# Kernel optimization log

Hardware: AMD Instinct MI355X
Metric: run time of the kernel (lower is better)

Reference implementation:

```python
import jax, jax.numpy as jnp
import numpy as np
from functools import partial

IN_DIM = 128
NUM_HEADS = 8
DOWN_DIM = IN_DIM // 2          # 64
HEAD_DIM = DOWN_DIM // NUM_HEADS  # 8
MID = max(1, DOWN_DIM // 16)    # 4 (gate_reduce=16)
DIL = 3
BN_EPS = 1e-5


def conv2d(x, w, padding=0, dilation=1):
    # x: [B,C,H,W], w: [O,I,kh,kw]
    return jax.lax.conv_general_dilated(
        x, w, window_strides=(1, 1),
        padding=[(padding, padding), (padding, padding)],
        rhs_dilation=(dilation, dilation),
        dimension_numbers=("NCHW", "OIHW", "NCHW"))


def batchnorm(x, gamma, beta, mean, var):
    # inference-mode BN over channel dim
    scale = (gamma / jnp.sqrt(var + BN_EPS))[None, :, None, None]
    shift = (beta - mean * gamma / jnp.sqrt(var + BN_EPS))[None, :, None, None]
    return x * scale + shift


def complex_l2_norm(z, eps=1e-6):
    denom = jnp.sqrt(jnp.sum(z.real ** 2 + z.imag ** 2, axis=-1, keepdims=True) + eps)
    return z / denom


def complex_softmax(z):
    return jax.lax.complex(jax.nn.softmax(z.real, axis=-1),
                           jax.nn.softmax(z.imag, axis=-1))


def setup_inputs() -> dict:
    key = jax.random.key(0)
    ks = jax.random.split(key, 6)
    B, H, W = 8, 128, 128
    inp = {}
    inp["x"] = jax.random.normal(ks[0], (B, IN_DIM, H, W), dtype=jnp.float32)
    inp["conv_w"] = jax.random.normal(ks[1], (DOWN_DIM, IN_DIM, 3, 3), dtype=jnp.float32) * 0.02
    inp["bn1_g"] = jnp.ones((DOWN_DIM,), jnp.float32)
    inp["bn1_b"] = jnp.zeros((DOWN_DIM,), jnp.float32)
    inp["bn1_m"] = jnp.zeros((DOWN_DIM,), jnp.float32)
    inp["bn1_v"] = jnp.ones((DOWN_DIM,), jnp.float32)
    inp["cg1_w"] = jax.random.normal(ks[2], (MID, DOWN_DIM, 1, 1), dtype=jnp.float32) * 0.1
    inp["cg1_b"] = jnp.zeros((MID,), jnp.float32)
    inp["cgbn_g"] = jnp.ones((MID,), jnp.float32)
    inp["cgbn_b"] = jnp.zeros((MID,), jnp.float32)
    inp["cgbn_m"] = jnp.zeros((MID,), jnp.float32)
    inp["cgbn_v"] = jnp.ones((MID,), jnp.float32)
    inp["cg2_w"] = jax.random.normal(ks[3], (DOWN_DIM, MID, 1, 1), dtype=jnp.float32) * 0.1
    inp["cg2_b"] = jnp.zeros((DOWN_DIM,), jnp.float32)
    inp["tau"] = jnp.ones((NUM_HEADS, 1, 1), jnp.float32) * (HEAD_DIM ** -0.5)
    return inp


def reference(x, conv_w, bn1_g, bn1_b, bn1_m, bn1_v,
              cg1_w, cg1_b, cgbn_g, cgbn_b, cgbn_m, cgbn_v,
              cg2_w, cg2_b, tau):
    B, C, H, W = x.shape
    # reduce branch: dilated 3x3 conv -> BN -> GELU (exact, matching torch nn.GELU)
    feat = conv2d(x, conv_w, padding=DIL, dilation=DIL)
    feat = batchnorm(feat, bn1_g, bn1_b, bn1_m, bn1_v)
    feat = jax.nn.gelu(feat, approximate=False)

    # q=k=v=g = fft2(feat) (torch computes four identical FFTs; same math)
    F2 = jnp.fft.fft2(feat.astype(jnp.float32), axes=(-2, -1))  # complex64 [B,64,H,W]
    N = H * W
    qkv = F2.reshape(B, NUM_HEADS, HEAD_DIM, N)  # b h d (H W)
    q = complex_l2_norm(qkv)
    k = complex_l2_norm(qkv)
    v = qkv
    # attn: [b,h,d,d] — tiny; contraction over N
    attn = jnp.einsum("bhdn,bhen->bhde", q, jnp.conj(k)) * tau
    attn = complex_softmax(attn)
    out_f = jnp.einsum("bhde,bhen->bhdn", attn, v)
    out_f = out_f.reshape(B, DOWN_DIM, H, W)
    out_f = jnp.abs(jnp.fft.ifft2(out_f, axes=(-2, -1)))

    # gated branch on g = F2
    gr = F2.real
    cg = conv2d(gr, cg1_w) + cg1_b[None, :, None, None]
    cg = batchnorm(cg, cgbn_g, cgbn_b, cgbn_m, cgbn_v)
    cg = jax.nn.gelu(cg, approximate=False)
    cg = conv2d(cg, cg2_w) + cg2_b[None, :, None, None]
    cg = jax.nn.sigmoid(cg)
    gate = cg * F2  # real gate times complex spectrum
    gate = jnp.abs(jnp.fft.ifft2(gate, axes=(-2, -1)))

    y = jnp.concatenate([out_f, gate], axis=1)
    return y + x
```

## Files before the change

### kernel.cpp

```cpp
#include <hip/hip_runtime.h>
#include <hip/hip_bf16.h>
#include <math.h>

#define NB 8
#define CIN 128
#define CDN 64
#define NPIX 16384
#define NHEADS 8
#define HDIM 8

typedef __attribute__((ext_vector_type(8))) short bf16x8;
typedef __attribute__((ext_vector_type(4))) float f32x4;
typedef __attribute__((ext_vector_type(8))) unsigned short u16x8;

struct alignas(8) c2 { float x, y; };

__device__ inline c2 cadd(c2 a, c2 b){ return {a.x+b.x, a.y+b.y}; }
__device__ inline c2 csub(c2 a, c2 b){ return {a.x-b.x, a.y-b.y}; }
__device__ inline c2 cmul(c2 a, c2 b){ return {a.x*b.x - a.y*b.y, a.x*b.y + a.y*b.x}; }
__device__ inline c2 shfl2(c2 v, int m){ return { __shfl_xor(v.x, m, 64), __shfl_xor(v.y, m, 64) }; }
__device__ inline float gelu_exact(float v){ return 0.5f*v*(1.f + erff(v*0.70710678118654752f)); }
__device__ inline unsigned short f2bf(float f){
  __hip_bfloat16 h = __float2bfloat16(f);
  return *reinterpret_cast<unsigned short*>(&h);
}
__device__ inline float bf2f(unsigned short u){ return __uint_as_float((unsigned)u << 16); }

struct Tw { c2 t0; c2 t[6]; };
__device__ inline void tw_init(Tw& w, int t){
  float sn, cs;
  sincosf(-6.283185307179586f * (float)t * (1.f/128.f), &sn, &cs); w.t0 = {cs, sn};
  #pragma unroll
  for (int i = 0; i < 6; ++i) {
    int sp = 32 >> i;
    int j = t & (sp-1);
    sincosf(-3.141592653589793f * (float)j / (float)sp, &sn, &cs);
    w.t[i] = {cs, sn};
  }
}
__device__ inline void fft128_fwd(c2& a, c2& b, int t, const Tw& w){
  c2 s = cadd(a,b), d = csub(a,b);
  a = s; b = cmul(d, w.t0);
  #pragma unroll
  for (int i = 0; i < 6; ++i) {
    int sp = 32 >> i;
    c2 oa = shfl2(a, sp), ob = shfl2(b, sp);
    c2 tw = w.t[i];
    if (t & sp) { a = cmul(csub(oa,a), tw); b = cmul(csub(ob,b), tw); }
    else        { a = cadd(a,oa);           b = cadd(b,ob); }
  }
}
__device__ inline void fft128_inv(c2& a, c2& b, int t, const Tw& w){
  #pragma unroll
  for (int i = 5; i >= 0; --i) {
    int sp = 32 >> i;
    c2 tw = {w.t[i].x, -w.t[i].y};
    c2 oa = shfl2(a, sp), ob = shfl2(b, sp);
    if (t & sp) { a = csub(oa, cmul(a, tw)); b = csub(ob, cmul(b, tw)); }
    else        { a = cadd(a, cmul(oa, tw)); b = cadd(b, cmul(ob, tw)); }
  }
  c2 t0c = {w.t0.x, -w.t0.y};
  c2 wb = cmul(b, t0c);
  b = csub(a, wb);
  a = cadd(a, wb);
}

__device__ inline void gload_lds16(const void* g, void* l){
  __builtin_amdgcn_global_load_lds(
      (const __attribute__((address_space(1))) unsigned int*)g,
      (__attribute__((address_space(3))) unsigned int*)l, 16, 0, 0);
}

__device__ inline int colmap8(int wv, int i){
  if (wv == 0) return i;
  if (wv == 1) return 8 + i;
  if (wv == 2) return i < 4 ? 16 + i : 24 + i;
  if (wv == 3) return 20 + i;
  if (wv < 8) { int a = wv - 4; return i < 4 ? 32 + 4*a + i : 56 - 4*a + i; }
  int a = wv - 8; return i < 4 ? 64 + 4*a + i : 120 - 4*a + i;
}

__global__ __launch_bounds__(256) void k_prep(const float* __restrict__ x, unsigned short* __restrict__ xT,
                                              const float* __restrict__ w, unsigned short* __restrict__ wP){
  if (blockIdx.x < 512) {
    int b = blockIdx.x >> 6;
    int px = (blockIdx.x & 63)*256 + threadIdx.x;
    const float* xb = x + (size_t)b*CIN*NPIX + px;
    #pragma unroll 2
    for (int ci0 = 0; ci0 < 128; ci0 += 8) {
      u16x8 v;
      #pragma unroll
      for (int j = 0; j < 8; ++j) v[j] = f2bf(xb[(size_t)(ci0+j)*NPIX]);
      int cc = ci0 >> 5;
      *(u16x8*)(xT + (((size_t)(b*4+cc)*NPIX + px)*32 + (ci0 & 31))) = v;
    }
  } else {
    int idx = (blockIdx.x - 512)*256 + threadIdx.x;
    if (idx >= 4*9*64*32) return;
    int cc  = idx / 18432;
    int r   = idx - cc*18432;
    int tap = r / 2048;
    int r2  = r - tap*2048;
    int co  = r2 >> 5;
    int cil = r2 & 31;
    int ci  = cc*32 + cil;
    wP[idx] = f2bf(w[(co*CIN + ci)*9 + tap]);
  }
}

__global__ __launch_bounds__(256) void k_conv(const unsigned short* __restrict__ xT,
    const unsigned short* __restrict__ wP,
    const float* __restrict__ bg, const float* __restrict__ bbeta,
    const float* __restrict__ bm, const float* __restrict__ bv,
    const float* __restrict__ w1,
    unsigned short* __restrict__ feat, float* __restrict__ u){
  __shared__ __align__(16) unsigned short sX[512*32];
  __shared__ float w1s[256];
  const int tid = threadIdx.x;
  const int flat = blockIdx.x + (blockIdx.y << 4) + (blockIdx.z << 7);
  const int half = (flat >> 3) & 1;
  const int tf   = (flat & 7) | ((flat >> 4) << 3);
  const int x0 = (tf & 7) * 16;
  const int y0 = ((tf >> 3) & 7) * 16;
  const int bb = tf >> 6;
  const int coBase = half*32;
  const int wv  = tid >> 6;
  const int l   = tid & 63;
  const int l15 = l & 15;
  const int g   = l >> 4;

  w1s[tid] = w1[tid];

  const bool interior = (x0 >= 16) && (x0 <= 96) && (y0 >= 16) && (y0 <= 96);

  f32x4 acc[2][4];
  #pragma unroll
  for (int m=0;m<2;++m)
    #pragma unroll
    for (int n=0;n<4;++n) acc[m][n] = {0.f,0.f,0.f,0.f};

  const int ko = g*8;

  for (int cc = 0; cc < 4; ++cc) {
    __syncthreads();
    const unsigned short* xcc = xT + ((size_t)(bb*4 + cc))*NPIX*32;
    if (interior) {
      #pragma unroll
      for (int k = 0; k < 8; ++k) {
        int blk = k*4 + wv;
        int idx = blk*64 + l;
        int p = idx >> 2, i = idx & 3;
        int pc = p < 484 ? p : 483;
        int py = pc / 22, px = pc - py*22;
        int gpix = (y0-3+py)*128 + (x0-3+px);
        int sg = i ^ ((p >> 1) & 3);
        const unsigned short* srcp = xcc + (size_t)gpix*32 + sg*8;
        gload_lds16(srcp, (char*)sX + blk*1024);
      }
    } else {
      #pragma unroll
      for (int k = 0; k < 8; ++k) {
        int idx = k*256 + tid;
        int p = idx >> 2, i = idx & 3;
        u16x8 v = {0,0,0,0,0,0,0,0};
        if (p < 484) {
          int py = p / 22, px = p - py*22;
          int gy = y0-3+py, gx = x0-3+px;
          if ((unsigned)gy < 128u && (unsigned)gx < 128u) {
            int sg = i ^ ((p >> 1) & 3);
            v = *(const u16x8*)(xcc + (size_t)(gy*128+gx)*32 + sg*8);
          }
        }
        *(u16x8*)((char*)sX + idx*16) = v;
      }
    }
    __syncthreads();

    const unsigned short* wcc = wP + cc*18432;
    for (int tap = 0; tap < 9; ++tap) {
      int dy = (tap/3)*3, dx = (tap - (tap/3)*3)*3;
      const unsigned short* wt = wcc + tap*2048;
      bf16x8 a[2], b[4];
      #pragma unroll
      for (int m = 0; m < 2; ++m)
        a[m] = *reinterpret_cast<const bf16x8*>(wt + (coBase + m*16 + l15)*32 + ko);
      #pragma unroll
      for (int n = 0; n < 4; ++n) {
        int p = (wv*4 + n + dy)*22 + l15 + dx;
        b[n] = *reinterpret_cast<const bf16x8*>(&sX[p*32 + ((g ^ ((p >> 1) & 3)) << 3)]);
      }
      #pragma unroll
      for (int m = 0; m < 2; ++m)
        #pragma unroll
        for (int n = 0; n < 4; ++n)
          acc[m][n] = __builtin_amdgcn_mfma_f32_16x16x32_bf16(a[m], b[n], acc[m][n], 0, 0, 0);
    }
  }

  float up[4][4];
  #pragma unroll
  for (int n=0;n<4;++n)
    #pragma unroll
    for (int m2=0;m2<4;++m2) up[n][m2] = 0.f;

  #pragma unroll
  for (int m = 0; m < 2; ++m) {
    #pragma unroll
    for (int r = 0; r < 4; ++r) {
      int co = coBase + m*16 + g*4 + r;
      float sc = bg[co] * rsqrtf(bv[co] + 1e-5f);
      float sh = bbeta[co] - bm[co]*sc;
      float wv4[4];
      #pragma unroll
      for (int m2 = 0; m2 < 4; ++m2) wv4[m2] = w1s[m2*64 + co];
      #pragma unroll
      for (int n = 0; n < 4; ++n) {
        int py = wv*4 + n;
        float v = gelu_exact(acc[m][n][r]*sc + sh);
        feat[((size_t)(bb*CDN + co)*128 + (y0+py))*128 + x0 + l15] = f2bf(v);
        #pragma unroll
        for (int m2 = 0; m2 < 4; ++m2) up[n][m2] += wv4[m2]*v;
      }
    }
  }
  #pragma unroll
  for (int n=0;n<4;++n)
    #pragma unroll
    for (int m2=0;m2<4;++m2) {
      up[n][m2] += __shfl_xor(up[n][m2], 16, 64);
      up[n][m2] += __shfl_xor(up[n][m2], 32, 64);
    }
  if (g == 0) {
    #pragma unroll
    for (int n = 0; n < 4; ++n) {
      int py = y0 + wv*4 + n;
      #pragma unroll
      for (int m2 = 0; m2 < 4; ++m2)
        u[((size_t)((bb*2 + half)*4 + m2))*NPIX + py*128 + x0 + l15] = up[n][m2];
    }
  }
}

__global__ __launch_bounds__(256) void k_attn1(const unsigned short* __restrict__ feat, float* __restrict__ part){
  int bh = blockIdx.x, ck = blockIdx.y;
  int b = bh >> 3, h = bh & 7;
  const unsigned short* f = feat + (size_t)(b*CDN + h*HDIM)*NPIX;
  float acc[36];
  #pragma unroll
  for (int i=0;i<36;++i) acc[i]=0.f;
  for (int p = ck*2048 + threadIdx.x; p < (ck+1)*2048; p += 256) {
    float v[8];
    #pragma unroll
    for (int d=0; d<8; ++d) v[d] = bf2f(f[d*NPIX + p]);
    int i = 0;
    #pragma unroll
    for (int d=0; d<8; ++d)
      #pragma unroll
      for (int e=0; e<=d; ++e) acc[i++] += v[d]*v[e];
  }
  #pragma unroll
  for (int i=0;i<36;++i)
    #pragma unroll
    for (int off=32; off; off>>=1) acc[i] += __shfl_xor(acc[i], off, 64);
  __shared__ float red[4][36];
  int wave = threadIdx.x >> 6, lane = threadIdx.x & 63;
  if (lane == 0) {
    #pragma unroll
    for (int i=0;i<36;++i) red[wave][i] = acc[i];
  }
  __syncthreads();
  if (threadIdx.x < 36)
    part[(bh*8+ck)*36 + threadIdx.x] =
      red[0][threadIdx.x]+red[1][threadIdx.x]+red[2][threadIdx.x]+red[3][threadIdx.x];
}

__global__ __launch_bounds__(256) void k_outf(const unsigned short* __restrict__ feat, const float* __restrict__ part,
                                              const float* __restrict__ tau,
                                              const float* __restrict__ x, float* __restrict__ out){
  int bh = blockIdx.x; int b = bh >> 3, h = bh & 7;
  int p = blockIdx.y*256 + threadIdx.x;
  __shared__ float A[64];
  __shared__ float Gm[36];
  if (threadIdx.x < 36) {
    float s = 0.f;
    #pragma unroll
    for (int k = 0; k < 8; ++k) s += part[(bh*8+k)*36 + threadIdx.x];
    Gm[threadIdx.x] = s;
  }
  __syncthreads();
  if (threadIdx.x == 0) {
    float G[8][8];
    int c=0;
    for (int d=0;d<8;++d) for(int e=0;e<=d;++e){
      float s = Gm[c]; G[d][e]=s; G[e][d]=s; ++c;
    }
    float nrm[8];
    for (int d=0;d<8;++d) nrm[d] = sqrtf(16384.f*G[d][d] + 1e-6f);
    float tv = tau[h];
    for (int d=0;d<8;++d) {
      float row[8]; float mx = -1e30f;
      for (int e=0;e<8;++e){ row[e] = tv*16384.f*G[d][e]/(nrm[d]*nrm[e]); mx = fmaxf(mx,row[e]); }
      float s=0.f;
      for (int e=0;e<8;++e){ row[e] = expf(row[e]-mx); s += row[e]; }
      for (int e=0;e<8;++e) A[d*8+e] = row[e]/s;
    }
  }
  __syncthreads();
  const unsigned short* f = feat + (size_t)(b*CDN + h*HDIM)*NPIX;
  float v[8];
  #pragma unroll
  for (int e=0;e<8;++e) v[e] = bf2f(f[e*NPIX + p]);
  float im = 0.f;
  #pragma unroll
  for (int e=0;e<8;++e) im += v[e];
  im *= 0.125f;
  #pragma unroll
  for (int d=0;d<8;++d){
    float re = 0.f;
    #pragma unroll
    for (int e=0;e<8;++e) re += A[d*8+e]*v[e];
    size_t o = ((size_t)(b*CIN + h*HDIM + d))*NPIX + p;
    out[o] = sqrtf(re*re + im*im) + x[o];
  }
}

__global__ __launch_bounds__(512) void k_ufft(const float* __restrict__ u,
    const float* __restrict__ b1,
    const float* __restrict__ gg, const float* __restrict__ gbeta,
    const float* __restrict__ gm, const float* __restrict__ gv,
    float* __restrict__ mid){
  __shared__ c2 T[64*129];
  int b = blockIdx.x >> 2, m = blockIdx.x & 3;
  int tid = threadIdx.x, wv = tid >> 6, t = tid & 63;
  Tw w; tw_init(w, t);
  const float* src0 = u + (size_t)((b*2+0)*4+m)*NPIX;
  const float* src1 = u + (size_t)((b*2+1)*4+m)*NPIX;
  c2 ra[16], rb[16];
  #pragma unroll
  for (int i = 0; i < 16; ++i) {
    int y = wv*16 + i;
    ra[i] = {src0[y*128 + t] + src1[y*128 + t], 0.f};
    rb[i] = {src0[y*128 + t + 64] + src1[y*128 + t + 64], 0.f};
  }
  #pragma unroll
  for (int i = 0; i < 16; ++i) fft128_fwd(ra[i], rb[i], t, w);
  c2 ca[16], cb[16];
  if (wv < 4) {
    #pragma unroll
    for (int i = 0; i < 16; ++i) {
      int y = wv*16 + i;
      T[y*129 + t] = ra[i]; T[y*129 + t + 64] = rb[i];
    }
  }
  __syncthreads();
  #pragma unroll
  for (int i = 0; i < 16; ++i) ca[i] = T[t*129 + wv*16 + i];
  __syncthreads();
  if (wv >= 4) {
    #pragma unroll
    for (int i = 0; i < 16; ++i) {
      int y = (wv-4)*16 + i;
      T[y*129 + t] = ra[i]; T[y*129 + t + 64] = rb[i];
    }
  }
  __syncthreads();
  #pragma unroll
  for (int i = 0; i < 16; ++i) cb[i] = T[t*129 + wv*16 + i];
  #pragma unroll
  for (int i = 0; i < 16; ++i) fft128_fwd(ca[i], cb[i], t, w);
  float sc = gg[m]*rsqrtf(gv[m]+1e-5f);
  float sh = gbeta[m] - gm[m]*sc;
  float bb1 = b1[m];
  float* md = mid + (size_t)(b*4+m)*NPIX;
  #pragma unroll
  for (int i = 0; i < 16; ++i) {
    int kx = wv*16 + i;
    md[kx*128 + t]      = gelu_exact((ca[i].x + bb1)*sc + sh);
    md[kx*128 + t + 64] = gelu_exact((cb[i].x + bb1)*sc + sh);
  }
}

__global__ __launch_bounds__(256) void k_gmap(const float* __restrict__ mid, const float* __restrict__ w2,
                                              const float* __restrict__ b2, unsigned* __restrict__ gPack){
  __shared__ float w2s[256], b2s[64];
  w2s[threadIdx.x] = w2[threadIdx.x];
  if (threadIdx.x < 64) b2s[threadIdx.x] = b2[threadIdx.x];
  __syncthreads();
  int b = blockIdx.x >> 6;
  int k = (blockIdx.x & 63)*256 + threadIdx.x;
  const float* md = mid + (size_t)b*4*NPIX + k;
  float m0 = md[0], m1 = md[NPIX], m2 = md[2*NPIX], m3 = md[3*NPIX];
  unsigned* gp = gPack + (size_t)b*32*NPIX + k;
  #pragma unroll 8
  for (int cp = 0; cp < 32; ++cp) {
    float slo = b2s[cp]    + w2s[cp*4]*m0    + w2s[cp*4+1]*m1    + w2s[cp*4+2]*m2    + w2s[cp*4+3]*m3;
    float shi = b2s[cp+32] + w2s[(cp+32)*4]*m0 + w2s[(cp+32)*4+1]*m1 + w2s[(cp+32)*4+2]*m2 + w2s[(cp+32)*4+3]*m3;
    slo = 1.f/(1.f+expf(-slo));
    shi = 1.f/(1.f+expf(-shi));
    gp[(size_t)cp*NPIX] = ((unsigned)f2bf(shi) << 16) | (unsigned)f2bf(slo);
  }
}

__global__ __launch_bounds__(1024)
void k_fused(const unsigned short* __restrict__ feat, const unsigned* __restrict__ gPack,
             const float* __restrict__ x, float* __restrict__ out){
  __shared__ c2 T[128*129];
  int ib = blockIdx.x;
  int b = ib >> 5, c = ib & 31;
  int tid = threadIdx.x, wv = tid >> 6, t = tid & 63;
  Tw w; tw_init(w, t);
  int ta = __brev((64 - (__brev(t) >> 26)) & 63) >> 26;
  const unsigned short* srcA = feat + (size_t)(b*CDN + c)*NPIX;
  const unsigned short* srcB = feat + (size_t)(b*CDN + c + 32)*NPIX;
  const unsigned* gp = gPack + (size_t)(b*32 + c)*NPIX;

  c2 ra[8], rb[8];
  #pragma unroll
  for (int i = 0; i < 8; ++i) {
    int y = wv*8 + i;
    ra[i] = {bf2f(srcA[y*128 + t]),      bf2f(srcB[y*128 + t])};
    rb[i] = {bf2f(srcA[y*128 + t + 64]), bf2f(srcB[y*128 + t + 64])};
  }
  #pragma unroll
  for (int i = 0; i < 8; ++i) fft128_fwd(ra[i], rb[i], t, w);
  #pragma unroll
  for (int i = 0; i < 8; ++i) {
    int y = wv*8 + i;
    T[y*129 + t] = ra[i]; T[y*129 + t + 64] = rb[i];
  }
  __syncthreads();
  c2 ca[8], cb[8];
  #pragma unroll
  for (int i = 0; i < 8; ++i) {
    int s = colmap8(wv, i);
    ca[i] = T[t*129 + s];
    cb[i] = T[(t+64)*129 + s];
  }
  unsigned gwa[8], gwb[8];
  #pragma unroll
  for (int i = 0; i < 8; ++i) {
    int s = colmap8(wv, i);
    gwa[i] = gp[s*128 + t];
    gwb[i] = gp[s*128 + 64 + t];
  }
  #pragma unroll
  for (int i = 0; i < 8; ++i) fft128_fwd(ca[i], cb[i], t, w);

  #define GUN(w_, lo_, hi_) float lo_ = __uint_as_float((w_) << 16); float hi_ = __uint_as_float((w_) & 0xffff0000u);
  #define CPAIR(I, J) { \
    GUN(gwa[I], g1aI, g2aI); GUN(gwb[I], g1bI, g2bI); \
    GUN(gwa[J], g1aJ, g2aJ); GUN(gwb[J], g1bJ, g2bJ); \
    c2 paI = { __shfl(ca[J].x, ta, 64), -__shfl(ca[J].y, ta, 64) }; \
    c2 paJ = { __shfl(ca[I].x, ta, 64), -__shfl(ca[I].y, ta, 64) }; \
    c2 pbI = { __shfl_xor(cb[J].x, 63, 64), -__shfl_xor(cb[J].y, 63, 64) }; \
    c2 pbJ = { __shfl_xor(cb[I].x, 63, 64), -__shfl_xor(cb[I].y, 63, 64) }; \
    float gsaI=0.5f*(g1aI+g2aI), gdaI=0.5f*(g1aI-g2aI); \
    float gsaJ=0.5f*(g1aJ+g2aJ), gdaJ=0.5f*(g1aJ-g2aJ); \
    float gsbI=0.5f*(g1bI+g2bI), gdbI=0.5f*(g1bI-g2bI); \
    float gsbJ=0.5f*(g1bJ+g2bJ), gdbJ=0.5f*(g1bJ-g2bJ); \
    ca[I] = { gsaI*ca[I].x + gdaI*paI.x, gsaI*ca[I].y + gdaI*paI.y }; \
    ca[J] = { gsaJ*ca[J].x + gdaJ*paJ.x, gsaJ*ca[J].y + gdaJ*paJ.y }; \
    cb[I] = { gsbI*cb[I].x + gdbI*pbI.x, gsbI*cb[I].y + gdbI*pbI.y }; \
    cb[J] = { gsbJ*cb[J].x + gdbJ*pbJ.x, gsbJ*cb[J].y + gdbJ*pbJ.y }; \
  }
  #define CSELF(I) { \
    GUN(gwa[I], g1aI, g2aI); GUN(gwb[I], g1bI, g2bI); \
    c2 paI = { __shfl(ca[I].x, ta, 64), -__shfl(ca[I].y, ta, 64) }; \
    c2 pbI = { __shfl_xor(cb[I].x, 63, 64), -__shfl_xor(cb[I].y, 63, 64) }; \
    float gsaI=0.5f*(g1aI+g2aI), gdaI=0.5f*(g1aI-g2aI); \
    float gsbI=0.5f*(g1bI+g2bI), gdbI=0.5f*(g1bI-g2bI); \
    ca[I] = { gsaI*ca[I].x + gdaI*paI.x, gsaI*ca[I].y + gdaI*paI.y }; \
    cb[I] = { gsbI*cb[I].x + gdbI*pbI.x, gsbI*cb[I].y + gdbI*pbI.y }; \
  }
  if (wv == 0) {
    CSELF(0); CSELF(1);
    CPAIR(2,3); CPAIR(4,7); CPAIR(5,6);
  } else {
    CPAIR(0,7); CPAIR(1,6); CPAIR(2,5); CPAIR(3,4);
  }
  #undef CPAIR
  #undef CSELF
  #undef GUN

  #pragma unroll
  for (int i = 0; i < 8; ++i) fft128_inv(ca[i], cb[i], t, w);
  __syncthreads();
  #pragma unroll
  for (int i = 0; i < 8; ++i) {
    int s = colmap8(wv, i);
    T[t*129 + s] = ca[i];
    T[(t+64)*129 + s] = cb[i];
  }
  __syncthreads();
  #pragma unroll
  for (int i = 0; i < 8; ++i) {
    int y = wv*8 + i;
    ra[i] = T[y*129 + t];
    rb[i] = T[y*129 + t + 64];
  }
  #pragma unroll
  for (int i = 0; i < 8; ++i) fft128_inv(ra[i], rb[i], t, w);
  const float* xr1 = x + ((size_t)(b*CIN + 64 + c))*NPIX;
  const float* xr2 = x + ((size_t)(b*CIN + 96 + c))*NPIX;
  float* o1 = out + ((size_t)(b*CIN + 64 + c))*NPIX;
  float* o2 = out + ((size_t)(b*CIN + 96 + c))*NPIX;
  const float s = 1.f/16384.f;
  #pragma unroll
  for (int i = 0; i < 8; ++i) {
    int y = wv*8 + i;
    o1[y*128 + t]      = fabsf(ra[i].x)*s + xr1[y*128 + t];
    o1[y*128 + t + 64] = fabsf(rb[i].x)*s + xr1[y*128 + t + 64];
    o2[y*128 + t]      = fabsf(ra[i].y)*s + xr2[y*128 + t];
    o2[y*128 + t + 64] = fabsf(rb[i].y)*s + xr2[y*128 + t + 64];
  }
}

extern "C" void kernel_launch(void* const* d_in, const int* in_sizes, int n_in,
                              void* d_out, int out_size, void* d_ws, size_t ws_size,
                              hipStream_t stream){
  const float* x      = (const float*)d_in[0];
  const float* conv_w = (const float*)d_in[1];
  const float* bn1_g  = (const float*)d_in[2];
  const float* bn1_b  = (const float*)d_in[3];
  const float* bn1_m  = (const float*)d_in[4];
  const float* bn1_v  = (const float*)d_in[5];
  const float* cg1_w  = (const float*)d_in[6];
  const float* cg1_b  = (const float*)d_in[7];
  const float* cgbn_g = (const float*)d_in[8];
  const float* cgbn_b = (const float*)d_in[9];
  const float* cgbn_m = (const float*)d_in[10];
  const float* cgbn_v = (const float*)d_in[11];
  const float* cg2_w  = (const float*)d_in[12];
  const float* cg2_b  = (const float*)d_in[13];
  const float* tau    = (const float*)d_in[14];
  float* out = (float*)d_out;

  char* ws = (char*)d_ws;
  unsigned short* feat  = (unsigned short*)ws;
  unsigned short* xT    = (unsigned short*)(ws + 33554432);
  unsigned*       gPack = (unsigned*)(ws + 33554432);
  float*          u     = (float*)(ws + 67108864);
  float*          mid   = (float*)(ws + 71303168);
  unsigned short* wPack = (unsigned short*)(ws + 73400320);
  float*          part  = (float*)(ws + 73547776);

  k_prep<<<800, 256, 0, stream>>>(x, xT, conv_w, wPack);
  k_conv<<<dim3(16,8,NB), 256, 0, stream>>>(xT, wPack, bn1_g, bn1_b, bn1_m, bn1_v, cg1_w, feat, u);
  k_ufft<<<NB*4, 512, 0, stream>>>(u, cg1_b, cgbn_g, cgbn_b, cgbn_m, cgbn_v, mid);
  k_gmap<<<NB*64, 256, 0, stream>>>(mid, cg2_w, cg2_b, gPack);
  k_attn1<<<dim3(NB*NHEADS, 8), 256, 0, stream>>>(feat, part);
  k_outf<<<dim3(NB*NHEADS, 64), 256, 0, stream>>>(feat, part, tau, x, out);
  k_fused<<<NB*32, 1024, 0, stream>>>(feat, gPack, x, out);
}
```

Baseline: 210.9 us.

## Split column FFT pass into two half-spectrum phases to halve LDS tile

The 128x129 complex LDS transpose buffer is replaced by a 128x65 buffer. The column pass now runs in two phases, one over column indices 0-63 and one over 64-127, each with its own column-to-wave map and conjugate-symmetric pairing. This halves shared memory per block (about 132KB down to 66KB) and the live column registers per phase, which may let more blocks reside per CU. In exchange it adds extra barriers and serializes the column work into two rounds.

Result: no change. 210.8 us (-0.0%).

```diff
diff --git a/kernel.cpp b/kernel.cpp
--- a/kernel.cpp
+++ b/kernel.cpp
@@ -71,13 +71,16 @@
       (__attribute__((address_space(3))) unsigned int*)l, 16, 0, 0);
 }
 
-__device__ inline int colmap8(int wv, int i){
+__device__ inline int cmapA(int wv, int i){
   if (wv == 0) return i;
-  if (wv == 1) return 8 + i;
-  if (wv == 2) return i < 4 ? 16 + i : 24 + i;
-  if (wv == 3) return 20 + i;
-  if (wv < 8) { int a = wv - 4; return i < 4 ? 32 + 4*a + i : 56 - 4*a + i; }
-  int a = wv - 8; return i < 4 ? 64 + 4*a + i : 120 - 4*a + i;
+  if (wv == 1) return 4 + i;
+  if (wv == 2) return i < 2 ? 8 + i : 12 + i;
+  if (wv == 3) return 10 + i;
+  if (wv < 8) { int a = wv - 4; return i < 2 ? 16 + 2*a + i : 28 - 2*a + i; }
+  int a = wv - 8; return i < 2 ? 32 + 2*a + i : 60 - 2*a + i;
+}
+__device__ inline int cmapB(int wv, int i){
+  return i < 2 ? 2*wv + i : 60 - 2*wv + i;
 }
 
 __global__ __launch_bounds__(256) void k_prep(const float* __restrict__ x, unsigned short* __restrict__ xT,
@@ -404,7 +407,7 @@
 __global__ __launch_bounds__(1024)
 void k_fused(const unsigned short* __restrict__ feat, const unsigned* __restrict__ gPack,
              const float* __restrict__ x, float* __restrict__ out){
-  __shared__ c2 T[128*129];
+  __shared__ c2 T[128*65];
   int ib = blockIdx.x;
   int b = ib >> 5, c = ib & 31;
   int tid = threadIdx.x, wv = tid >> 6, t = tid & 63;
@@ -423,28 +426,6 @@
   }
   #pragma unroll
   for (int i = 0; i < 8; ++i) fft128_fwd(ra[i], rb[i], t, w);
-  #pragma unroll
-  for (int i = 0; i < 8; ++i) {
-    int y = wv*8 + i;
-    T[y*129 + t] = ra[i]; T[y*129 + t + 64] = rb[i];
-  }
-  __syncthreads();
-  c2 ca[8], cb[8];
-  #pragma unroll
-  for (int i = 0; i < 8; ++i) {
-    int s = colmap8(wv, i);
-    ca[i] = T[t*129 + s];
-    cb[i] = T[(t+64)*129 + s];
-  }
-  unsigned gwa[8], gwb[8];
-  #pragma unroll
-  for (int i = 0; i < 8; ++i) {
-    int s = colmap8(wv, i);
-    gwa[i] = gp[s*128 + t];
-    gwb[i] = gp[s*128 + 64 + t];
-  }
-  #pragma unroll
-  for (int i = 0; i < 8; ++i) fft128_fwd(ca[i], cb[i], t, w);
 
   #define GUN(w_, lo_, hi_) float lo_ = __uint_as_float((w_) << 16); float hi_ = __uint_as_float((w_) & 0xffff0000u);
   #define CPAIR(I, J) { \
@@ -472,32 +453,60 @@
     ca[I] = { gsaI*ca[I].x + gdaI*paI.x, gsaI*ca[I].y + gdaI*paI.y }; \
     cb[I] = { gsbI*cb[I].x + gdbI*pbI.x, gsbI*cb[I].y + gdbI*pbI.y }; \
   }
-  if (wv == 0) {
-    CSELF(0); CSELF(1);
-    CPAIR(2,3); CPAIR(4,7); CPAIR(5,6);
-  } else {
-    CPAIR(0,7); CPAIR(1,6); CPAIR(2,5); CPAIR(3,4);
-  }
+
+  #pragma unroll
+  for (int i = 0; i < 8; ++i) T[(wv*8 + i)*65 + t] = ra[i];
+  __syncthreads();
+  {
+    int s0 = cmapA(wv,0), s1 = cmapA(wv,1), s2 = cmapA(wv,2), s3 = cmapA(wv,3);
+    c2 ca[4], cb[4];
+    ca[0]=T[t*65+s0]; ca[1]=T[t*65+s1]; ca[2]=T[t*65+s2]; ca[3]=T[t*65+s3];
+    cb[0]=T[(t+64)*65+s0]; cb[1]=T[(t+64)*65+s1]; cb[2]=T[(t+64)*65+s2]; cb[3]=T[(t+64)*65+s3];
+    unsigned gwa[4], gwb[4];
+    gwa[0]=gp[s0*128+t]; gwa[1]=gp[s1*128+t]; gwa[2]=gp[s2*128+t]; gwa[3]=gp[s3*128+t];
+    gwb[0]=gp[s0*128+64+t]; gwb[1]=gp[s1*128+64+t]; gwb[2]=gp[s2*128+64+t]; gwb[3]=gp[s3*128+64+t];
+    #pragma unroll
+    for (int j = 0; j < 4; ++j) fft128_fwd(ca[j], cb[j], t, w);
+    if (wv == 0) { CSELF(0); CSELF(1); CPAIR(2,3); }
+    else         { CPAIR(0,3); CPAIR(1,2); }
+    #pragma unroll
+    for (int j = 0; j < 4; ++j) fft128_inv(ca[j], cb[j], t, w);
+    __syncthreads();
+    T[t*65+s0]=ca[0]; T[t*65+s1]=ca[1]; T[t*65+s2]=ca[2]; T[t*65+s3]=ca[3];
+    T[(t+64)*65+s0]=cb[0]; T[(t+64)*65+s1]=cb[1]; T[(t+64)*65+s2]=cb[2]; T[(t+64)*65+s3]=cb[3];
+  }
+  __syncthreads();
+  #pragma unroll
+  for (int i = 0; i < 8; ++i) ra[i] = T[(wv*8 + i)*65 + t];
+  __syncthreads();
+
+  #pragma unroll
+  for (int i = 0; i < 8; ++i) T[(wv*8 + i)*65 + t] = rb[i];
+  __syncthreads();
+  {
+    int s0 = cmapB(wv,0), s1 = cmapB(wv,1), s2 = cmapB(wv,2), s3 = cmapB(wv,3);
+    c2 ca[4], cb[4];
+    ca[0]=T[t*65+s0]; ca[1]=T[t*65+s1]; ca[2]=T[t*65+s2]; ca[3]=T[t*65+s3];
+    cb[0]=T[(t+64)*65+s0]; cb[1]=T[(t+64)*65+s1]; cb[2]=T[(t+64)*65+s2]; cb[3]=T[(t+64)*65+s3];
+    unsigned gwa[4], gwb[4];
+    gwa[0]=gp[(64+s0)*128+t]; gwa[1]=gp[(64+s1)*128+t]; gwa[2]=gp[(64+s2)*128+t]; gwa[3]=gp[(64+s3)*128+t];
+    gwb[0]=gp[(64+s0)*128+64+t]; gwb[1]=gp[(64+s1)*128+64+t]; gwb[2]=gp[(64+s2)*128+64+t]; gwb[3]=gp[(64+s3)*128+64+t];
+    #pragma unroll
+    for (int j = 0; j < 4; ++j) fft128_fwd(ca[j], cb[j], t, w);
+    CPAIR(0,3); CPAIR(1,2);
+    #pragma unroll
+    for (int j = 0; j < 4; ++j) fft128_inv(ca[j], cb[j], t, w);
+    __syncthreads();
+    T[t*65+s0]=ca[0]; T[t*65+s1]=ca[1]; T[t*65+s2]=ca[2]; T[t*65+s3]=ca[3];
+    T[(t+64)*65+s0]=cb[0]; T[(t+64)*65+s1]=cb[1]; T[(t+64)*65+s2]=cb[2]; T[(t+64)*65+s3]=cb[3];
+  }
+  __syncthreads();
+  #pragma unroll
+  for (int i = 0; i < 8; ++i) rb[i] = T[(wv*8 + i)*65 + t];
   #undef CPAIR
   #undef CSELF
   #undef GUN
 
-  #pragma unroll
-  for (int i = 0; i < 8; ++i) fft128_inv(ca[i], cb[i], t, w);
-  __syncthreads();
-  #pragma unroll
-  for (int i = 0; i < 8; ++i) {
-    int s = colmap8(wv, i);
-    T[t*129 + s] = ca[i];
-    T[(t+64)*129 + s] = cb[i];
-  }
-  __syncthreads();
-  #pragma unroll
-  for (int i = 0; i < 8; ++i) {
-    int y = wv*8 + i;
-    ra[i] = T[y*129 + t];
-    rb[i] = T[y*129 + t + 64];
-  }
   #pragma unroll
   for (int i = 0; i < 8; ++i) fft128_inv(ra[i], rb[i], t, w);
   const float* xr1 = x + ((size_t)(b*CIN + 64 + c))*NPIX;
```
